# Optimization experiments

Hardware: AMD Instinct MI355X
Metric: run time of the kernel (lower is better)

Reference implementation:

```python
import jax, jax.numpy as jnp
import numpy as np

N_NODES = 50000
N_EDGES = 600000
N_GRAPHS = 256
BN_EPS = 1e-5
NEG_SLOPE = 0.2  # PyG GATv2 default leaky_relu slope


def segment_softmax(logits, seg, num_segments):
    # logits: [E, H], softmax over edges sharing the same destination node
    m = jax.ops.segment_max(logits, seg, num_segments=num_segments)
    e = jnp.exp(logits - m[seg])
    s = jax.ops.segment_sum(e, seg, num_segments=num_segments)
    return e / (s[seg] + 1e-16)


def gatv2_layer(h, edge_attr, src, dst, Wl, bl, Wr, br, We, att, bias, concat):
    # PyG GATv2Conv (share_weights=False, edge_dim set), eval mode (no dropout)
    heads, out_c = att.shape
    N = h.shape[0]
    xl = (h @ Wl + bl).reshape(N, heads, out_c)  # messages from source
    xr = (h @ Wr + br).reshape(N, heads, out_c)  # destination term
    em = (edge_attr @ We).reshape(-1, heads, out_c)
    z = jax.nn.leaky_relu(xl[src] + xr[dst] + em, NEG_SLOPE)  # [E,H,C]
    logits = jnp.einsum('ehc,hc->eh', z, att)
    alpha = segment_softmax(logits, dst, N)  # [E,H]
    out = jax.ops.segment_sum(xl[src] * alpha[:, :, None], dst, num_segments=N)
    out = out.reshape(N, heads * out_c) if concat else out.mean(axis=1)
    return out + bias


def batch_norm(h, gamma, beta):
    mu = h.mean(axis=0)
    var = h.var(axis=0)
    return gamma * (h - mu) * jax.lax.rsqrt(var + BN_EPS) + beta


def setup_inputs() -> dict:
    key = jax.random.key(0)
    ks = jax.random.split(key, 32)
    F, Fe, H, C = 64, 16, 4, 64
    HC = H * C

    def w(k, shape):
        return jax.random.normal(k, shape, dtype=jnp.float32) * 0.1

    inp = {
        'x': jax.random.normal(ks[0], (N_NODES, F), dtype=jnp.float32),
        'edge_attr': jax.random.normal(ks[1], (N_EDGES, Fe), dtype=jnp.float32),
        'edge_index': jax.random.randint(ks[2], (2, N_EDGES), 0, N_NODES, dtype=jnp.int32),
        'batch': jnp.sort(jax.random.randint(ks[3], (N_NODES,), 0, N_GRAPHS, dtype=jnp.int32)),
        # input projection
        'W_in': w(ks[4], (F, C)), 'b_in': jnp.zeros((C,), jnp.float32),
        'Wl0': w(ks[5], (C, HC)), 'bl0': jnp.zeros((HC,), jnp.float32),
        'Wr0': w(ks[6], (C, HC)), 'br0': jnp.zeros((HC,), jnp.float32),
        'We0': w(ks[7], (Fe, HC)),
        'att0': w(ks[8], (H, C)), 'bias0': jnp.zeros((HC,), jnp.float32),
        'g0': jnp.ones((HC,), jnp.float32), 'beta0': jnp.zeros((HC,), jnp.float32),
        'Wl1': w(ks[9], (HC, HC)), 'bl1': jnp.zeros((HC,), jnp.float32),
        'Wr1': w(ks[10], (HC, HC)), 'br1': jnp.zeros((HC,), jnp.float32),
        'We1': w(ks[11], (Fe, HC)),
        'att1': w(ks[12], (H, C)), 'bias1': jnp.zeros((C,), jnp.float32),
        'g1': jnp.ones((C,), jnp.float32), 'beta1': jnp.zeros((C,), jnp.float32),
        # MLP head 64 -> 32 -> 16 -> 1
        'Wm1': w(ks[13], (C, C // 2)), 'bm1': jnp.zeros((C // 2,), jnp.float32),
        'Wm2': w(ks[14], (C // 2, C // 4)), 'bm2': jnp.zeros((C // 4,), jnp.float32),
        'Wm3': w(ks[15], (C // 4, 1)), 'bm3': jnp.zeros((1,), jnp.float32),
    }
    return inp


def reference(x, edge_attr, W_in, b_in,
              Wl0, bl0, Wr0, br0, We0, att0, bias0, g0, beta0,
              Wl1, bl1, Wr1, br1, We1, att1, bias1, g1, beta1,
              Wm1, bm1, Wm2, bm2, Wm3, bm3,
              edge_index, batch):
    src, dst = edge_index[0], edge_index[1]
    h = jax.nn.relu(x @ W_in + b_in)
    h = gatv2_layer(h, edge_attr, src, dst, Wl0, bl0, Wr0, br0, We0, att0, bias0, True)
    h = batch_norm(h, g0, beta0)
    h = jax.nn.relu(h)  # dropout is identity in eval mode
    h = gatv2_layer(h, edge_attr, src, dst, Wl1, bl1, Wr1, br1, We1, att1, bias1, False)
    h = batch_norm(h, g1, beta1)
    # global mean pool over graphs
    cnt = jax.ops.segment_sum(jnp.ones((h.shape[0],), h.dtype), batch, num_segments=N_GRAPHS)
    pooled = jax.ops.segment_sum(h, batch, num_segments=N_GRAPHS) / jnp.maximum(cnt, 1.0)[:, None]
    z = jax.nn.relu(pooled @ Wm1 + bm1)
    z = jax.nn.relu(z @ Wm2 + bm2)
    return z @ Wm3 + bm3  # [N_GRAPHS, 1]
```

## Files before the change

kernel.cpp:

```cpp
#include <hip/hip_runtime.h>
#include <math.h>

constexpr int NN = 50000;
constexpr int NE = 600000;
constexpr int NG = 256;
constexpr int SB = (NN + 255) / 256;
constexpr float kBnEps = 1e-5f;
constexpr float kSlope = 0.2f;

__device__ __forceinline__ float rdlane(float v, int l) {
    return __builtin_bit_cast(float, __builtin_amdgcn_readlane(__builtin_bit_cast(int, v), l));
}

template <int CTRL>
__device__ __forceinline__ float dppadd(float v) {
    int t = __builtin_amdgcn_mov_dpp(__builtin_bit_cast(int, v), CTRL, 0xF, 0xF, true);
    return v + __builtin_bit_cast(float, t);
}
__device__ __forceinline__ float sum16(float v) {
    v = dppadd<0xB1>(v);
    v = dppadd<0x4E>(v);
    v = dppadd<0x141>(v);
    v = dppadd<0x140>(v);
    return v;
}

__device__ __forceinline__ float4 fma4(float a, float4 b, float4 c) {
    c.x = fmaf(a, b.x, c.x); c.y = fmaf(a, b.y, c.y);
    c.z = fmaf(a, b.z, c.z); c.w = fmaf(a, b.w, c.w);
    return c;
}

__global__ __launch_bounds__(256) void k_input_proj(
    const float* __restrict__ x, const float* __restrict__ W,
    const float* __restrict__ b, float* __restrict__ h0)
{
    __shared__ float Wl[64 * 64];
    __shared__ float bl[64];
    int tid = threadIdx.x;
    for (int i = tid; i < 64 * 64; i += 256) Wl[i] = W[i];
    if (tid < 64) bl[tid] = b[tid];
    __syncthreads();
    int lane = tid & 63, wave = tid >> 6;
    int row = blockIdx.x * 4 + wave;
    if (row >= NN) return;
    float xv = x[(size_t)row * 64 + lane];
    float acc = bl[lane];
    #pragma unroll
    for (int k = 0; k < 64; ++k) {
        float hb = rdlane(xv, k);
        acc = fmaf(hb, Wl[k * 64 + lane], acc);
    }
    h0[(size_t)row * 64 + lane] = fmaxf(acc, 0.f);
}

__global__ __launch_bounds__(256) void k_hist(const int* __restrict__ dst, int* __restrict__ cnt)
{
    int e = blockIdx.x * 256 + threadIdx.x;
    if (e < NE) atomicAdd(&cnt[dst[e]], 1);
}

__global__ __launch_bounds__(256) void k_scanA(const int* __restrict__ cnt,
                                               int* __restrict__ offs, int* __restrict__ bsum)
{
    __shared__ int s[256];
    int tid = threadIdx.x;
    int i = blockIdx.x * 256 + tid;
    int v = (i < NN) ? cnt[i] : 0;
    s[tid] = v;
    __syncthreads();
    #pragma unroll
    for (int d = 1; d < 256; d <<= 1) {
        int u = (tid >= d) ? s[tid - d] : 0;
        __syncthreads();
        s[tid] += u;
        __syncthreads();
    }
    if (i < NN) offs[i] = s[tid];
    if (tid == 255) bsum[blockIdx.x] = s[255];
}

__global__ __launch_bounds__(256) void k_scanB(int* __restrict__ bsum)
{
    __shared__ int s[256];
    int t = threadIdx.x;
    int v = (t < SB) ? bsum[t] : 0;
    s[t] = v;
    __syncthreads();
    #pragma unroll
    for (int d = 1; d < 256; d <<= 1) {
        int u = (t >= d) ? s[t - d] : 0;
        __syncthreads();
        s[t] += u;
        __syncthreads();
    }
    if (t < SB) bsum[t] = s[t];
}

__global__ __launch_bounds__(256) void k_scanC(const int* __restrict__ cnt,
                                               const int* __restrict__ bsum,
                                               int* __restrict__ offs, int* __restrict__ cur)
{
    int i = blockIdx.x * 256 + threadIdx.x;
    if (i > NN) return;
    if (i == NN) { offs[NN] = NE; return; }
    int pre = (blockIdx.x > 0) ? bsum[blockIdx.x - 1] : 0;
    int v = offs[i] - cnt[i] + pre;
    offs[i] = v;
    cur[i] = v;
}

__global__ __launch_bounds__(256) void k_scatter(const int* __restrict__ dst,
                                                 const int* __restrict__ src,
                                                 const float* __restrict__ ea,
                                                 int* __restrict__ cur,
                                                 int* __restrict__ srcs,
                                                 float* __restrict__ eas)
{
    int e = blockIdx.x * 256 + threadIdx.x;
    if (e < NE) {
        int p = atomicAdd(&cur[dst[e]], 1);
        srcs[p] = src[e];
        const float4* s4 = (const float4*)(ea + (size_t)e * 16);
        float4* d4 = (float4*)(eas + (size_t)p * 16);
        d4[0] = s4[0]; d4[1] = s4[1]; d4[2] = s4[2]; d4[3] = s4[3];
    }
}

__global__ __launch_bounds__(256) void k_gbounds(const int* __restrict__ batch,
                                                 int* __restrict__ gstart)
{
    int g = threadIdx.x;
    int lo = 0, hi = NN;
    while (lo < hi) {
        int mid = (lo + hi) >> 1;
        if (batch[mid] < g) lo = mid + 1; else hi = mid;
    }
    gstart[g] = lo;
    if (g == 0) gstart[NG] = NN;
}

template <int K, bool BN>
__global__ __launch_bounds__(256) void k_linear2(
    const float* __restrict__ h, const float* __restrict__ WL,
    const float* __restrict__ WR, const float* __restrict__ bl,
    const float* __restrict__ br, const float* __restrict__ scale,
    const float* __restrict__ shift, float* __restrict__ outl,
    float* __restrict__ outr)
{
    int tid = threadIdx.x;
    int lane = tid & 63, wave = tid >> 6;
    int row0 = blockIdx.x * 32 + wave * 8;
    int q = lane >> 4;
    int kl = lane & 15;
    float4 accL[8], accR[8];
    #pragma unroll
    for (int r = 0; r < 8; ++r) {
        accL[r] = make_float4(0.f, 0.f, 0.f, 0.f);
        accR[r] = make_float4(0.f, 0.f, 0.f, 0.f);
    }

    for (int kt = 0; kt < K / 16; ++kt) {
        float hreg[2];
        float sc = 1.f, sh = 0.f;
        if (BN) { sc = scale[kt * 16 + kl]; sh = shift[kt * 16 + kl]; }
        #pragma unroll
        for (int r = 0; r < 2; ++r) {
            int row = row0 + 4 * r + q;
            if (row >= NN) row = NN - 1;
            float v = h[(size_t)row * K + kt * 16 + kl];
            if (BN) v = fmaxf(fmaf(v, sc, sh), 0.f);
            hreg[r] = v;
        }
        #pragma unroll
        for (int k = 0; k < 16; ++k) {
            float4 wl4 = ((const float4*)(WL + (size_t)(kt * 16 + k) * 256))[lane];
            float4 wr4 = ((const float4*)(WR + (size_t)(kt * 16 + k) * 256))[lane];
            #pragma unroll
            for (int j = 0; j < 8; ++j) {
                float hb = rdlane(hreg[j >> 2], (j & 3) * 16 + k);
                accL[j] = fma4(hb, wl4, accL[j]);
                accR[j] = fma4(hb, wr4, accR[j]);
            }
        }
    }
    float4 bl4 = ((const float4*)bl)[lane];
    float4 br4 = ((const float4*)br)[lane];
    #pragma unroll
    for (int j = 0; j < 8; ++j) {
        int row = row0 + j;
        if (row < NN) {
            float4 o;
            o.x = accL[j].x + bl4.x; o.y = accL[j].y + bl4.y;
            o.z = accL[j].z + bl4.z; o.w = accL[j].w + bl4.w;
            ((float4*)(outl + (size_t)row * 256))[lane] = o;
            float4 pp;
            pp.x = accR[j].x + br4.x; pp.y = accR[j].y + br4.y;
            pp.z = accR[j].z + br4.z; pp.w = accR[j].w + br4.w;
            ((float4*)(outr + (size_t)row * 256))[lane] = pp;
        }
    }
}

template <bool CONCAT, int NPW>
__global__ __launch_bounds__(256) void k_attn(
    const float* __restrict__ xl, const float* __restrict__ xr,
    const float* __restrict__ eas, const float* __restrict__ We,
    const float* __restrict__ att, const int* __restrict__ srcs,
    const int* __restrict__ offs, const float* __restrict__ bias,
    float* __restrict__ out)
{
    int tid = threadIdx.x;
    int lane = tid & 63, wave = tid >> 6;
    float4 wr[16];
    #pragma unroll
    for (int k = 0; k < 16; ++k) wr[k] = ((const float4*)(We + k * 256))[lane];
    float4 ar = ((const float4*)att)[lane];

    int g16 = lane >> 4;
    int k16 = lane & 15;
    int nodebase = (blockIdx.x * 4 + wave) * NPW;
    if (nodebase >= NN) return;

    for (int nn = 0; nn < NPW; ++nn) {
        int n = nodebase + nn;
        if (n >= NN) break;
        int beg = offs[n], end = offs[n + 1];
        float4 xr4 = ((const float4*)(xr + (size_t)n * 256))[lane];

        float m = -INFINITY, ssum = 0.f;
        float4 acc = make_float4(0.f, 0.f, 0.f, 0.f);

        float nea = 0.f;
        float4 nx0, nx1, nx2, nx3;

        auto loadbatch = [&](int i) {
            int idx = i + g16;
            if (idx > end - 1) idx = end - 1;
            nea = eas[(size_t)idx * 16 + k16];
            int sv = srcs[idx];
            int s0 = __builtin_amdgcn_readlane(sv, 0);
            int s1 = __builtin_amdgcn_readlane(sv, 16);
            int s2 = __builtin_amdgcn_readlane(sv, 32);
            int s3 = __builtin_amdgcn_readlane(sv, 48);
            nx0 = ((const float4*)(xl + (size_t)s0 * 256))[lane];
            nx1 = ((const float4*)(xl + (size_t)s1 * 256))[lane];
            nx2 = ((const float4*)(xl + (size_t)s2 * 256))[lane];
            nx3 = ((const float4*)(xl + (size_t)s3 * 256))[lane];
        };

        if (beg < end) loadbatch(beg);

        for (int i = beg; i < end; i += 4) {
            float cea = nea;
            float4 x0 = nx0, x1 = nx1, x2 = nx2, x3 = nx3;
            if (i + 4 < end) loadbatch(i + 4);

            float p[4];
            #pragma unroll
            for (int g = 0; g < 4; ++g) {
                float4 xg = (g == 0) ? x0 : (g == 1) ? x1 : (g == 2) ? x2 : x3;
                float4 em = xr4;
                #pragma unroll
                for (int k = 0; k < 16; ++k) {
                    float a = rdlane(cea, g * 16 + k);
                    em.x = fmaf(a, wr[k].x, em.x);
                    em.y = fmaf(a, wr[k].y, em.y);
                    em.z = fmaf(a, wr[k].z, em.z);
                    em.w = fmaf(a, wr[k].w, em.w);
                }
                float z0 = xg.x + em.x;
                float z1 = xg.y + em.y;
                float z2 = xg.z + em.z;
                float z3 = xg.w + em.w;
                z0 = (z0 > 0.f) ? z0 : kSlope * z0;
                z1 = (z1 > 0.f) ? z1 : kSlope * z1;
                z2 = (z2 > 0.f) ? z2 : kSlope * z2;
                z3 = (z3 > 0.f) ? z3 : kSlope * z3;
                float pv = fmaf(z0, ar.x, fmaf(z1, ar.y, fmaf(z2, ar.z, z3 * ar.w)));
                pv = sum16(pv);
                p[g] = (i + g < end) ? pv : -INFINITY;
            }
            float pm = fmaxf(fmaxf(p[0], p[1]), fmaxf(p[2], p[3]));
            float mn = fmaxf(m, pm);
            float sc = __expf(m - mn);
            float w0 = __expf(p[0] - mn);
            float w1 = __expf(p[1] - mn);
            float w2 = __expf(p[2] - mn);
            float w3 = __expf(p[3] - mn);
            ssum = fmaf(ssum, sc, (w0 + w1) + (w2 + w3));
            acc.x = fmaf(acc.x, sc, fmaf(w0, x0.x, fmaf(w1, x1.x, fmaf(w2, x2.x, w3 * x3.x))));
            acc.y = fmaf(acc.y, sc, fmaf(w0, x0.y, fmaf(w1, x1.y, fmaf(w2, x2.y, w3 * x3.y))));
            acc.z = fmaf(acc.z, sc, fmaf(w0, x0.z, fmaf(w1, x1.z, fmaf(w2, x2.z, w3 * x3.z))));
            acc.w = fmaf(acc.w, sc, fmaf(w0, x0.w, fmaf(w1, x1.w, fmaf(w2, x2.w, w3 * x3.w))));
            m = mn;
        }

        float inv = 1.f / (ssum + 1e-16f);
        if (CONCAT) {
            float4 b4 = ((const float4*)bias)[lane];
            float4 o;
            o.x = fmaf(acc.x, inv, b4.x);
            o.y = fmaf(acc.y, inv, b4.y);
            o.z = fmaf(acc.z, inv, b4.z);
            o.w = fmaf(acc.w, inv, b4.w);
            ((float4*)(out + (size_t)n * 256))[lane] = o;
        } else {
            float v0 = acc.x * inv, v1 = acc.y * inv, v2 = acc.z * inv, v3 = acc.w * inv;
            v0 += __shfl_xor(v0, 16, 64); v0 += __shfl_xor(v0, 32, 64);
            v1 += __shfl_xor(v1, 16, 64); v1 += __shfl_xor(v1, 32, 64);
            v2 += __shfl_xor(v2, 16, 64); v2 += __shfl_xor(v2, 32, 64);
            v3 += __shfl_xor(v3, 16, 64); v3 += __shfl_xor(v3, 32, 64);
            if (lane < 16) {
                float4 b4 = ((const float4*)bias)[lane];
                float4 o;
                o.x = fmaf(0.25f, v0, b4.x);
                o.y = fmaf(0.25f, v1, b4.y);
                o.z = fmaf(0.25f, v2, b4.z);
                o.w = fmaf(0.25f, v3, b4.w);
                ((float4*)(out + (size_t)n * 64))[lane] = o;
            }
        }
    }
}

template <int CH>
__global__ __launch_bounds__(256) void k_bn_stats(const float* __restrict__ h,
                                                  float* __restrict__ sum,
                                                  float* __restrict__ sumsq)
{
    constexpr int RP = 256 / CH;
    int tid = threadIdx.x;
    int c = tid % CH;
    int rsub = tid / CH;
    float s = 0.f, q = 0.f;
    for (int n = blockIdx.x * RP + rsub; n < NN; n += gridDim.x * RP) {
        float v = h[(size_t)n * CH + c];
        s += v; q = fmaf(v, v, q);
    }
    __shared__ float ls[256], lq[256];
    ls[tid] = s; lq[tid] = q;
    __syncthreads();
    if (tid < CH) {
        #pragma unroll
        for (int r = 1; r < RP; ++r) { s += ls[tid + r * CH]; q += lq[tid + r * CH]; }
        atomicAdd(&sum[tid], s);
        atomicAdd(&sumsq[tid], q);
    }
}

__global__ void k_bn_finalize(const float* __restrict__ sum, const float* __restrict__ sumsq,
                              const float* __restrict__ g, const float* __restrict__ beta,
                              float* __restrict__ scale, float* __restrict__ shift, int CH)
{
    int c = threadIdx.x;
    if (c >= CH) return;
    float inv_n = 1.f / (float)NN;
    float mu = sum[c] * inv_n;
    float var = sumsq[c] * inv_n - mu * mu;
    float sc = g[c] / sqrtf(var + kBnEps);
    scale[c] = sc;
    shift[c] = fmaf(-mu, sc, beta[c]);
}

__global__ __launch_bounds__(256) void k_pool_mlp(
    const float* __restrict__ h2, const float* __restrict__ scale,
    const float* __restrict__ shift, const int* __restrict__ gstart,
    const float* __restrict__ Wm1, const float* __restrict__ bm1,
    const float* __restrict__ Wm2, const float* __restrict__ bm2,
    const float* __restrict__ Wm3, const float* __restrict__ bm3,
    float* __restrict__ out)
{
    int g = blockIdx.x, tid = threadIdx.x;
    int lane = tid & 63, wave = tid >> 6;
    int s = gstart[g], e = gstart[g + 1];
    float sc = scale[lane], sh = shift[lane];
    float acc = 0.f;
    for (int n = s + wave; n < e; n += 4)
        acc += fmaf(h2[(size_t)n * 64 + lane], sc, sh);
    __shared__ float red[4][64];
    red[wave][lane] = acc;
    __syncthreads();
    __shared__ float p[64], z1[32], z2[16];
    if (tid < 64) {
        float cnt = (float)(e - s);
        float a = red[0][tid] + red[1][tid] + red[2][tid] + red[3][tid];
        p[tid] = a / fmaxf(cnt, 1.f);
    }
    __syncthreads();
    if (tid < 32) {
        float a = bm1[tid];
        #pragma unroll
        for (int k = 0; k < 64; ++k) a = fmaf(p[k], Wm1[k * 32 + tid], a);
        z1[tid] = fmaxf(a, 0.f);
    }
    __syncthreads();
    if (tid < 16) {
        float a = bm2[tid];
        #pragma unroll
        for (int k = 0; k < 32; ++k) a = fmaf(z1[k], Wm2[k * 16 + tid], a);
        z2[tid] = fmaxf(a, 0.f);
    }
    __syncthreads();
    if (tid == 0) {
        float a = bm3[0];
        #pragma unroll
        for (int k = 0; k < 16; ++k) a = fmaf(z2[k], Wm3[k], a);
        out[g] = a;
    }
}

extern "C" void kernel_launch(void* const* d_in, const int* in_sizes, int n_in,
                              void* d_out, int out_size, void* d_ws, size_t ws_size,
                              hipStream_t stream)
{
    const float* x     = (const float*)d_in[0];
    const float* ea    = (const float*)d_in[1];
    const int*   ei    = (const int*)d_in[2];
    const int*   bat   = (const int*)d_in[3];
    const float* W_in  = (const float*)d_in[4];
    const float* b_in  = (const float*)d_in[5];
    const float* Wl0   = (const float*)d_in[6];
    const float* bl0   = (const float*)d_in[7];
    const float* Wr0   = (const float*)d_in[8];
    const float* br0   = (const float*)d_in[9];
    const float* We0   = (const float*)d_in[10];
    const float* att0  = (const float*)d_in[11];
    const float* bias0 = (const float*)d_in[12];
    const float* g0    = (const float*)d_in[13];
    const float* beta0 = (const float*)d_in[14];
    const float* Wl1   = (const float*)d_in[15];
    const float* bl1   = (const float*)d_in[16];
    const float* Wr1   = (const float*)d_in[17];
    const float* br1   = (const float*)d_in[18];
    const float* We1   = (const float*)d_in[19];
    const float* att1  = (const float*)d_in[20];
    const float* bias1 = (const float*)d_in[21];
    const float* g1    = (const float*)d_in[22];
    const float* beta1 = (const float*)d_in[23];
    const float* Wm1   = (const float*)d_in[24];
    const float* bm1   = (const float*)d_in[25];
    const float* Wm2   = (const float*)d_in[26];
    const float* bm2   = (const float*)d_in[27];
    const float* Wm3   = (const float*)d_in[28];
    const float* bm3   = (const float*)d_in[29];
    const int* src = ei;
    const int* dst = ei + NE;
    float* out = (float*)d_out;

    char* p = (char*)d_ws;
    auto take = [&](size_t nbytes) -> char* {
        char* q = p;
        p += (nbytes + 255) & ~(size_t)255;
        return q;
    };
    char* z0 = p;
    int*   hist   = (int*)take((size_t)NN * 4);
    float* bns0   = (float*)take(256 * 4);
    float* bnq0   = (float*)take(256 * 4);
    float* bns1   = (float*)take(64 * 4);
    float* bnq1   = (float*)take(64 * 4);
    size_t zbytes = (size_t)(p - z0);
    int*   offs   = (int*)take((size_t)(NN + 1) * 4);
    int*   curs   = (int*)take((size_t)NN * 4);
    int*   bsum   = (int*)take((size_t)SB * 4);
    int*   gstart = (int*)take((size_t)(NG + 1) * 4);
    int*   srcs   = (int*)take((size_t)NE * 4);
    float* eas    = (float*)take((size_t)NE * 16 * 4);
    float* h0     = (float*)take((size_t)NN * 64 * 4);
    float* xl     = (float*)take((size_t)NN * 256 * 4);
    float* xr     = (float*)take((size_t)NN * 256 * 4);
    float* h1     = (float*)take((size_t)NN * 256 * 4);
    float* scale0 = (float*)take(256 * 4);
    float* shift0 = (float*)take(256 * 4);
    float* scale1 = (float*)take(64 * 4);
    float* shift1 = (float*)take(64 * 4);

    hipMemsetAsync(z0, 0, zbytes, stream);

    k_input_proj<<<(NN + 3) / 4, 256, 0, stream>>>(x, W_in, b_in, h0);

    k_hist<<<(NE + 255) / 256, 256, 0, stream>>>(dst, hist);
    k_scanA<<<SB, 256, 0, stream>>>(hist, offs, bsum);
    k_scanB<<<1, 256, 0, stream>>>(bsum);
    k_scanC<<<SB, 256, 0, stream>>>(hist, bsum, offs, curs);
    k_scatter<<<(NE + 255) / 256, 256, 0, stream>>>(dst, src, ea, curs, srcs, eas);
    k_gbounds<<<1, 256, 0, stream>>>(bat, gstart);

    constexpr int NPW = 2;
    int attn_blocks = (NN + 4 * NPW - 1) / (4 * NPW);
    int lin_blocks = (NN + 31) / 32;

    k_linear2<64, false><<<lin_blocks, 256, 0, stream>>>(
        h0, Wl0, Wr0, bl0, br0, nullptr, nullptr, xl, xr);
    k_attn<true, NPW><<<attn_blocks, 256, 0, stream>>>(
        xl, xr, eas, We0, att0, srcs, offs, bias0, h1);
    k_bn_stats<256><<<256, 256, 0, stream>>>(h1, bns0, bnq0);
    k_bn_finalize<<<1, 256, 0, stream>>>(bns0, bnq0, g0, beta0, scale0, shift0, 256);

    k_linear2<256, true><<<lin_blocks, 256, 0, stream>>>(
        h1, Wl1, Wr1, bl1, br1, scale0, shift0, xl, xr);
    k_attn<false, NPW><<<attn_blocks, 256, 0, stream>>>(
        xl, xr, eas, We1, att1, srcs, offs, bias1, h0);
    k_bn_stats<64><<<256, 256, 0, stream>>>(h0, bns1, bnq1);
    k_bn_finalize<<<1, 64, 0, stream>>>(bns1, bnq1, g1, beta1, scale1, shift1, 64);

    k_pool_mlp<<<NG, 256, 0, stream>>>(h0, scale1, shift1, gstart,
                                       Wm1, bm1, Wm2, bm2, Wm3, bm3, out);
}
```

Measured before the change: 816.6 us.

## Fuse input projection into layer-0 linear, prefetch in linear2, double-buffer attention gathers

Merges the input projection into the first GATv2 linear kernel so h0 is computed in registers and never written to memory. Moves the graph-boundary binary search into the pool kernel, removing one launch. Adds software prefetch of the next K-tile of activations and BN params in k_linear2. Processes edges in two interleaved batches of four in the attention kernel so more gather loads are in flight. The cost is more registers and some redundant per-block work.

After: 861.1 us. +5.4%, slower.

```diff
diff --git a/kernel.cpp b/kernel.cpp
--- a/kernel.cpp
+++ b/kernel.cpp
@@ -29,29 +29,6 @@
     c.x = fmaf(a, b.x, c.x); c.y = fmaf(a, b.y, c.y);
     c.z = fmaf(a, b.z, c.z); c.w = fmaf(a, b.w, c.w);
     return c;
-}
-
-__global__ __launch_bounds__(256) void k_input_proj(
-    const float* __restrict__ x, const float* __restrict__ W,
-    const float* __restrict__ b, float* __restrict__ h0)
-{
-    __shared__ float Wl[64 * 64];
-    __shared__ float bl[64];
-    int tid = threadIdx.x;
-    for (int i = tid; i < 64 * 64; i += 256) Wl[i] = W[i];
-    if (tid < 64) bl[tid] = b[tid];
-    __syncthreads();
-    int lane = tid & 63, wave = tid >> 6;
-    int row = blockIdx.x * 4 + wave;
-    if (row >= NN) return;
-    float xv = x[(size_t)row * 64 + lane];
-    float acc = bl[lane];
-    #pragma unroll
-    for (int k = 0; k < 64; ++k) {
-        float hb = rdlane(xv, k);
-        acc = fmaf(hb, Wl[k * 64 + lane], acc);
-    }
-    h0[(size_t)row * 64 + lane] = fmaxf(acc, 0.f);
 }
 
 __global__ __launch_bounds__(256) void k_hist(const int* __restrict__ dst, int* __restrict__ cnt)
@@ -127,61 +104,49 @@
     }
 }
 
-__global__ __launch_bounds__(256) void k_gbounds(const int* __restrict__ batch,
-                                                 int* __restrict__ gstart)
-{
-    int g = threadIdx.x;
-    int lo = 0, hi = NN;
-    while (lo < hi) {
-        int mid = (lo + hi) >> 1;
-        if (batch[mid] < g) lo = mid + 1; else hi = mid;
-    }
-    gstart[g] = lo;
-    if (g == 0) gstart[NG] = NN;
-}
-
-template <int K, bool BN>
-__global__ __launch_bounds__(256) void k_linear2(
-    const float* __restrict__ h, const float* __restrict__ WL,
+__global__ __launch_bounds__(256) void k_lin0(
+    const float* __restrict__ x, const float* __restrict__ Win,
+    const float* __restrict__ bin, const float* __restrict__ WL,
     const float* __restrict__ WR, const float* __restrict__ bl,
-    const float* __restrict__ br, const float* __restrict__ scale,
-    const float* __restrict__ shift, float* __restrict__ outl,
+    const float* __restrict__ br, float* __restrict__ outl,
     float* __restrict__ outr)
 {
     int tid = threadIdx.x;
     int lane = tid & 63, wave = tid >> 6;
     int row0 = blockIdx.x * 32 + wave * 8;
-    int q = lane >> 4;
-    int kl = lane & 15;
+
+    float xreg[8];
+    #pragma unroll
+    for (int j = 0; j < 8; ++j) {
+        int row = row0 + j; if (row >= NN) row = NN - 1;
+        xreg[j] = x[(size_t)row * 64 + lane];
+    }
+    float h0r[8];
+    float b0 = bin[lane];
+    #pragma unroll
+    for (int j = 0; j < 8; ++j) h0r[j] = b0;
+    for (int k = 0; k < 64; ++k) {
+        float w = Win[k * 64 + lane];
+        #pragma unroll
+        for (int j = 0; j < 8; ++j) h0r[j] = fmaf(rdlane(xreg[j], k), w, h0r[j]);
+    }
+    #pragma unroll
+    for (int j = 0; j < 8; ++j) h0r[j] = fmaxf(h0r[j], 0.f);
+
     float4 accL[8], accR[8];
     #pragma unroll
-    for (int r = 0; r < 8; ++r) {
-        accL[r] = make_float4(0.f, 0.f, 0.f, 0.f);
-        accR[r] = make_float4(0.f, 0.f, 0.f, 0.f);
-    }
-
-    for (int kt = 0; kt < K / 16; ++kt) {
-        float hreg[2];
-        float sc = 1.f, sh = 0.f;
-        if (BN) { sc = scale[kt * 16 + kl]; sh = shift[kt * 16 + kl]; }
-        #pragma unroll
-        for (int r = 0; r < 2; ++r) {
-            int row = row0 + 4 * r + q;
-            if (row >= NN) row = NN - 1;
-            float v = h[(size_t)row * K + kt * 16 + kl];
-            if (BN) v = fmaxf(fmaf(v, sc, sh), 0.f);
-            hreg[r] = v;
-        }
-        #pragma unroll
-        for (int k = 0; k < 16; ++k) {
-            float4 wl4 = ((const float4*)(WL + (size_t)(kt * 16 + k) * 256))[lane];
-            float4 wr4 = ((const float4*)(WR + (size_t)(kt * 16 + k) * 256))[lane];
-            #pragma unroll
-            for (int j = 0; j < 8; ++j) {
-                float hb = rdlane(hreg[j >> 2], (j & 3) * 16 + k);
-                accL[j] = fma4(hb, wl4, accL[j]);
-                accR[j] = fma4(hb, wr4, accR[j]);
-            }
+    for (int j = 0; j < 8; ++j) {
+        accL[j] = make_float4(0.f, 0.f, 0.f, 0.f);
+        accR[j] = make_float4(0.f, 0.f, 0.f, 0.f);
+    }
+    for (int k = 0; k < 64; ++k) {
+        float4 wl4 = ((const float4*)(WL + (size_t)k * 256))[lane];
+        float4 wr4 = ((const float4*)(WR + (size_t)k * 256))[lane];
+        #pragma unroll
+        for (int j = 0; j < 8; ++j) {
+            float hb = rdlane(h0r[j], k);
+            accL[j] = fma4(hb, wl4, accL[j]);
+            accR[j] = fma4(hb, wr4, accR[j]);
         }
     }
     float4 bl4 = ((const float4*)bl)[lane];
@@ -202,6 +167,75 @@
     }
 }
 
+template <int K, bool BN>
+__global__ __launch_bounds__(256) void k_linear2(
+    const float* __restrict__ h, const float* __restrict__ WL,
+    const float* __restrict__ WR, const float* __restrict__ bl,
+    const float* __restrict__ br, const float* __restrict__ scale,
+    const float* __restrict__ shift, float* __restrict__ outl,
+    float* __restrict__ outr)
+{
+    int tid = threadIdx.x;
+    int lane = tid & 63, wave = tid >> 6;
+    int row0 = blockIdx.x * 32 + wave * 8;
+    int q = lane >> 4;
+    int kl = lane & 15;
+    float4 accL[8], accR[8];
+    #pragma unroll
+    for (int r = 0; r < 8; ++r) {
+        accL[r] = make_float4(0.f, 0.f, 0.f, 0.f);
+        accR[r] = make_float4(0.f, 0.f, 0.f, 0.f);
+    }
+
+    int rowA = row0 + q;     if (rowA >= NN) rowA = NN - 1;
+    int rowB = row0 + 4 + q; if (rowB >= NN) rowB = NN - 1;
+    const float* hA = h + (size_t)rowA * K;
+    const float* hB = h + (size_t)rowB * K;
+
+    float rawA = hA[kl], rawB = hB[kl];
+    float scv = BN ? scale[kl] : 1.f, shv = BN ? shift[kl] : 0.f;
+
+    for (int kt = 0; kt < K / 16; ++kt) {
+        float hreg[2];
+        hreg[0] = BN ? fmaxf(fmaf(rawA, scv, shv), 0.f) : rawA;
+        hreg[1] = BN ? fmaxf(fmaf(rawB, scv, shv), 0.f) : rawB;
+        float nrA = 0.f, nrB = 0.f, nsc = 1.f, nsh = 0.f;
+        if (kt + 1 < K / 16) {
+            int o = (kt + 1) * 16 + kl;
+            nrA = hA[o]; nrB = hB[o];
+            if (BN) { nsc = scale[o]; nsh = shift[o]; }
+        }
+        #pragma unroll
+        for (int k = 0; k < 16; ++k) {
+            float4 wl4 = ((const float4*)(WL + (size_t)(kt * 16 + k) * 256))[lane];
+            float4 wr4 = ((const float4*)(WR + (size_t)(kt * 16 + k) * 256))[lane];
+            #pragma unroll
+            for (int j = 0; j < 8; ++j) {
+                float hb = rdlane(hreg[j >> 2], (j & 3) * 16 + k);
+                accL[j] = fma4(hb, wl4, accL[j]);
+                accR[j] = fma4(hb, wr4, accR[j]);
+            }
+        }
+        rawA = nrA; rawB = nrB; scv = nsc; shv = nsh;
+    }
+    float4 bl4 = ((const float4*)bl)[lane];
+    float4 br4 = ((const float4*)br)[lane];
+    #pragma unroll
+    for (int j = 0; j < 8; ++j) {
+        int row = row0 + j;
+        if (row < NN) {
+            float4 o;
+            o.x = accL[j].x + bl4.x; o.y = accL[j].y + bl4.y;
+            o.z = accL[j].z + bl4.z; o.w = accL[j].w + bl4.w;
+            ((float4*)(outl + (size_t)row * 256))[lane] = o;
+            float4 pp;
+            pp.x = accR[j].x + br4.x; pp.y = accR[j].y + br4.y;
+            pp.z = accR[j].z + br4.z; pp.w = accR[j].w + br4.w;
+            ((float4*)(outr + (size_t)row * 256))[lane] = pp;
+        }
+    }
+}
+
 template <bool CONCAT, int NPW>
 __global__ __launch_bounds__(256) void k_attn(
     const float* __restrict__ xl, const float* __restrict__ xr,
@@ -231,10 +265,10 @@
         float m = -INFINITY, ssum = 0.f;
         float4 acc = make_float4(0.f, 0.f, 0.f, 0.f);
 
-        float nea = 0.f;
-        float4 nx0, nx1, nx2, nx3;
-
-        auto loadbatch = [&](int i) {
+        float neaA = 0.f, neaB = 0.f;
+        float4 nxA0, nxA1, nxA2, nxA3, nxB0, nxB1, nxB2, nxB3;
+
+        auto ldsrc = [&](int i, float& nea, float4& n0, float4& n1, float4& n2, float4& n3) {
             int idx = i + g16;
             if (idx > end - 1) idx = end - 1;
             nea = eas[(size_t)idx * 16 + k16];
@@ -243,19 +277,13 @@
             int s1 = __builtin_amdgcn_readlane(sv, 16);
             int s2 = __builtin_amdgcn_readlane(sv, 32);
             int s3 = __builtin_amdgcn_readlane(sv, 48);
-            nx0 = ((const float4*)(xl + (size_t)s0 * 256))[lane];
-            nx1 = ((const float4*)(xl + (size_t)s1 * 256))[lane];
-            nx2 = ((const float4*)(xl + (size_t)s2 * 256))[lane];
-            nx3 = ((const float4*)(xl + (size_t)s3 * 256))[lane];
+            n0 = ((const float4*)(xl + (size_t)s0 * 256))[lane];
+            n1 = ((const float4*)(xl + (size_t)s1 * 256))[lane];
+            n2 = ((const float4*)(xl + (size_t)s2 * 256))[lane];
+            n3 = ((const float4*)(xl + (size_t)s3 * 256))[lane];
         };
 
-        if (beg < end) loadbatch(beg);
-
-        for (int i = beg; i < end; i += 4) {
-            float cea = nea;
-            float4 x0 = nx0, x1 = nx1, x2 = nx2, x3 = nx3;
-            if (i + 4 < end) loadbatch(i + 4);
-
+        auto process = [&](int i, float cea, float4 x0, float4 x1, float4 x2, float4 x3) {
             float p[4];
             #pragma unroll
             for (int g = 0; g < 4; ++g) {
@@ -294,6 +322,24 @@
             acc.z = fmaf(acc.z, sc, fmaf(w0, x0.z, fmaf(w1, x1.z, fmaf(w2, x2.z, w3 * x3.z))));
             acc.w = fmaf(acc.w, sc, fmaf(w0, x0.w, fmaf(w1, x1.w, fmaf(w2, x2.w, w3 * x3.w))));
             m = mn;
+        };
+
+        if (beg < end) ldsrc(beg, neaA, nxA0, nxA1, nxA2, nxA3);
+        if (beg + 4 < end) ldsrc(beg + 4, neaB, nxB0, nxB1, nxB2, nxB3);
+
+        for (int i = beg; i < end; i += 8) {
+            {
+                float cea = neaA;
+                float4 c0 = nxA0, c1 = nxA1, c2 = nxA2, c3 = nxA3;
+                if (i + 8 < end) ldsrc(i + 8, neaA, nxA0, nxA1, nxA2, nxA3);
+                process(i, cea, c0, c1, c2, c3);
+            }
+            if (i + 4 < end) {
+                float cea = neaB;
+                float4 c0 = nxB0, c1 = nxB1, c2 = nxB2, c3 = nxB3;
+                if (i + 12 < end) ldsrc(i + 12, neaB, nxB0, nxB1, nxB2, nxB3);
+                process(i + 4, cea, c0, c1, c2, c3);
+            }
         }
 
         float inv = 1.f / (ssum + 1e-16f);
@@ -365,7 +411,7 @@
 
 __global__ __launch_bounds__(256) void k_pool_mlp(
     const float* __restrict__ h2, const float* __restrict__ scale,
-    const float* __restrict__ shift, const int* __restrict__ gstart,
+    const float* __restrict__ shift, const int* __restrict__ batch,
     const float* __restrict__ Wm1, const float* __restrict__ bm1,
     const float* __restrict__ Wm2, const float* __restrict__ bm2,
     const float* __restrict__ Wm3, const float* __restrict__ bm3,
@@ -373,7 +419,18 @@
 {
     int g = blockIdx.x, tid = threadIdx.x;
     int lane = tid & 63, wave = tid >> 6;
-    int s = gstart[g], e = gstart[g + 1];
+    __shared__ int sb[2];
+    if (tid < 2) {
+        int target = g + tid;
+        int lo = 0, hi = NN;
+        while (lo < hi) {
+            int mid = (lo + hi) >> 1;
+            if (batch[mid] < target) lo = mid + 1; else hi = mid;
+        }
+        sb[tid] = lo;
+    }
+    __syncthreads();
+    int s = sb[0], e = sb[1];
     float sc = scale[lane], sh = shift[lane];
     float acc = 0.f;
     for (int n = s + wave; n < e; n += 4)
@@ -464,10 +521,9 @@
     int*   offs   = (int*)take((size_t)(NN + 1) * 4);
     int*   curs   = (int*)take((size_t)NN * 4);
     int*   bsum   = (int*)take((size_t)SB * 4);
-    int*   gstart = (int*)take((size_t)(NG + 1) * 4);
     int*   srcs   = (int*)take((size_t)NE * 4);
     float* eas    = (float*)take((size_t)NE * 16 * 4);
-    float* h0     = (float*)take((size_t)NN * 64 * 4);
+    float* h2     = (float*)take((size_t)NN * 64 * 4);
     float* xl     = (float*)take((size_t)NN * 256 * 4);
     float* xr     = (float*)take((size_t)NN * 256 * 4);
     float* h1     = (float*)take((size_t)NN * 256 * 4);
@@ -478,21 +534,18 @@
 
     hipMemsetAsync(z0, 0, zbytes, stream);
 
-    k_input_proj<<<(NN + 3) / 4, 256, 0, stream>>>(x, W_in, b_in, h0);
-
     k_hist<<<(NE + 255) / 256, 256, 0, stream>>>(dst, hist);
     k_scanA<<<SB, 256, 0, stream>>>(hist, offs, bsum);
     k_scanB<<<1, 256, 0, stream>>>(bsum);
     k_scanC<<<SB, 256, 0, stream>>>(hist, bsum, offs, curs);
     k_scatter<<<(NE + 255) / 256, 256, 0, stream>>>(dst, src, ea, curs, srcs, eas);
-    k_gbounds<<<1, 256, 0, stream>>>(bat, gstart);
 
     constexpr int NPW = 2;
     int attn_blocks = (NN + 4 * NPW - 1) / (4 * NPW);
     int lin_blocks = (NN + 31) / 32;
 
-    k_linear2<64, false><<<lin_blocks, 256, 0, stream>>>(
-        h0, Wl0, Wr0, bl0, br0, nullptr, nullptr, xl, xr);
+    k_lin0<<<lin_blocks, 256, 0, stream>>>(
+        x, W_in, b_in, Wl0, Wr0, bl0, br0, xl, xr);
     k_attn<true, NPW><<<attn_blocks, 256, 0, stream>>>(
         xl, xr, eas, We0, att0, srcs, offs, bias0, h1);
     k_bn_stats<256><<<256, 256, 0, stream>>>(h1, bns0, bnq0);
@@ -501,10 +554,10 @@
     k_linear2<256, true><<<lin_blocks, 256, 0, stream>>>(
         h1, Wl1, Wr1, bl1, br1, scale0, shift0, xl, xr);
     k_attn<false, NPW><<<attn_blocks, 256, 0, stream>>>(
-        xl, xr, eas, We1, att1, srcs, offs, bias1, h0);
-    k_bn_stats<64><<<256, 256, 0, stream>>>(h0, bns1, bnq1);
+        xl, xr, eas, We1, att1, srcs, offs, bias1, h2);
+    k_bn_stats<64><<<256, 256, 0, stream>>>(h2, bns1, bnq1);
     k_bn_finalize<<<1, 64, 0, stream>>>(bns1, bnq1, g1, beta1, scale1, shift1, 64);
 
-    k_pool_mlp<<<NG, 256, 0, stream>>>(h0, scale1, shift1, gstart,
+    k_pool_mlp<<<NG, 256, 0, stream>>>(h2, scale1, shift1, bat,
                                        Wm1, bm1, Wm2, bm2, Wm3, bm3, out);
 }
```
